# Performance work log

Measured on AMD Instinct MI355X. Metric: run time of the kernel, lower is better.

The kernel has to match this reference:

```python
import jax, jax.numpy as jnp
import numpy as np

DIM = 128
N = 4096


def setup_inputs() -> dict:
    key = jax.random.key(0)
    ks = jax.random.split(key, 12)
    d = DIM
    s = 0.02
    inp = jax.random.normal(ks[0], (N, 2 * d), dtype=jnp.float32)
    # H = myLinear: (2d -> 5d -> 1), tanh after each layer
    Hw1 = jax.random.normal(ks[1], (2 * d, 5 * d), dtype=jnp.float32) * s
    Hb1 = jax.random.normal(ks[2], (5 * d,), dtype=jnp.float32) * s
    Hw2 = jax.random.normal(ks[3], (5 * d, 1), dtype=jnp.float32) * s
    Hb2 = jax.random.normal(ks[4], (1,), dtype=jnp.float32) * s
    # augment_f: (d -> 4d -> 8d -> d*d), tanh after each layer
    Aw1 = jax.random.normal(ks[5], (d, 4 * d), dtype=jnp.float32) * s
    Ab1 = jax.random.normal(ks[6], (4 * d,), dtype=jnp.float32) * s
    Aw2 = jax.random.normal(ks[7], (4 * d, 8 * d), dtype=jnp.float32) * s
    Ab2 = jax.random.normal(ks[8], (8 * d,), dtype=jnp.float32) * s
    Aw3 = jax.random.normal(ks[9], (8 * d, d * d), dtype=jnp.float32) * s
    Ab3 = jax.random.normal(ks[10], (d * d,), dtype=jnp.float32) * s
    u = jax.random.uniform(ks[11], (d,), dtype=jnp.float32, minval=-0.001, maxval=0.001)
    return {"t": 0, "inp": inp, "Hw1": Hw1, "Hb1": Hb1, "Hw2": Hw2, "Hb2": Hb2,
            "Aw1": Aw1, "Ab1": Ab1, "Aw2": Aw2, "Ab2": Ab2, "Aw3": Aw3, "Ab3": Ab3, "u": u}


def reference(t, inp, Hw1, Hb1, Hw2, Hb2, Aw1, Ab1, Aw2, Ab2, Aw3, Ab3, u):
    d = DIM
    n = inp.shape[0]

    def H_scalar(z):  # z: [2d] -> scalar
        h = jnp.tanh(z @ Hw1 + Hb1)
        return jnp.tanh(h @ Hw2 + Hb2)[0]

    # per-sample gradient of scalar H w.r.t. input (== batch_jacobian squeeze)
    g = jax.vmap(jax.grad(H_scalar))(inp)  # [N, 2d]
    dx = g[:, :d]
    dv = -g[:, d:]

    x = inp[:, :d]
    h1 = jnp.tanh(x @ Aw1 + Ab1)            # [N, 4d]
    h2 = jnp.tanh(h1 @ Aw2 + Ab2)           # [N, 8d]
    gq = jnp.tanh(h2 @ Aw3 + Ab3).reshape(n, d, d)  # [N, d, d]
    dv = dv + jnp.einsum("nij,j->ni", gq, u)
    return jnp.concatenate([dx, dv], axis=-1)  # [N, 2d]
```

## Files before the change

### kernel.cpp

```cpp
#include <hip/hip_runtime.h>
#include <hip/hip_bf16.h>
#include <cstdint>


typedef __bf16 bf16_t;
typedef __bf16 bf16x4_t __attribute__((ext_vector_type(4)));
typedef __bf16 bf16x8_t __attribute__((ext_vector_type(8)));
typedef float f32x4_t __attribute__((ext_vector_type(4)));
typedef float f32x16_t __attribute__((ext_vector_type(16)));
typedef int intx4_t __attribute__((ext_vector_type(4)));
typedef int intx8_t __attribute__((ext_vector_type(8)));

#define DIMD 128
#define NROW 4096
#define SMEM_BYTES 18432
#define SMEM3_BYTES 26624

__device__ __forceinline__ float fast_tanh(float x) {
  float t = __builtin_amdgcn_exp2f(x * 2.8853900817779268f);
  return 1.f - 2.f * __builtin_amdgcn_rcpf(t + 1.f);
}

__device__ __forceinline__ uint8_t to_fp8(float x) {
  return (uint8_t)(__builtin_amdgcn_cvt_pk_fp8_f32(x, x, 0, false) & 0xff);
}

__device__ __forceinline__ void g2l16(const void* gp, void* lp) {
  __builtin_amdgcn_global_load_lds(
      reinterpret_cast<__attribute__((address_space(1))) void*>(
          reinterpret_cast<uintptr_t>(gp)),
      reinterpret_cast<__attribute__((address_space(3))) void*>(
          reinterpret_cast<uintptr_t>(lp)),
      16, 0, 0);
}

template <int EPI>
__device__ __forceinline__ void gemm_body(char* smem, int bx, int by,
                                          const bf16_t* A, int lda,
                                          const bf16_t* B, int ldb, int K,
                                          const float* bias, void* outp,
                                          int ldo) {
  constexpr int BK = 32;
  bf16_t* As = (bf16_t*)smem;
  bf16_t* Bs = As + 4096;

  const int m0 = bx * 128;
  const int n0 = by * 128;
  const int tid = threadIdx.x;
  const int wave = tid >> 6;
  const int lane = tid & 63;
  const int wm = wave >> 1;
  const int wn = wave & 1;

  const int sr = lane >> 2;
  const int sk = (((lane & 3) ^ ((sr >> 1) & 3)) * 8);
  const int fr = lane & 15;
  const int fk = (((lane >> 4) ^ ((fr >> 1) & 3)) * 8);

  f32x4_t acc[4][4] = {};

  for (int k0 = 0; k0 < K; k0 += BK) {
    if (k0) __syncthreads();
#pragma unroll
    for (int t = 0; t < 2; ++t) {
      const int rb = wave * 32 + t * 16;
      g2l16(A + (size_t)(m0 + rb + sr) * lda + (k0 + sk), As + rb * BK);
      g2l16(B + (size_t)(n0 + rb + sr) * ldb + (k0 + sk), Bs + rb * BK);
    }
    __syncthreads();

    bf16x8_t af[4], bb[4];
#pragma unroll
    for (int t = 0; t < 4; ++t) {
      af[t] = *(const bf16x8_t*)(As + (wm * 64 + t * 16 + fr) * BK + fk);
      bb[t] = *(const bf16x8_t*)(Bs + (wn * 64 + t * 16 + fr) * BK + fk);
    }
#pragma unroll
    for (int i = 0; i < 4; ++i)
#pragma unroll
      for (int j = 0; j < 4; ++j)
        acc[i][j] = __builtin_amdgcn_mfma_f32_16x16x32_bf16(af[i], bb[j],
                                                            acc[i][j], 0, 0, 0);
  }

  if constexpr (EPI == 0) {
    bf16_t* O = (bf16_t*)outp;
#pragma unroll
    for (int i = 0; i < 4; ++i) {
      const int row = m0 + wm * 64 + i * 16 + (lane >> 4) * 4;
#pragma unroll
      for (int j = 0; j < 4; ++j) {
        const int col = n0 + wn * 64 + j * 16 + fr;
        const float b = bias[col];
#pragma unroll
        for (int r = 0; r < 4; ++r)
          O[(size_t)(row + r) * ldo + col] = (bf16_t)fast_tanh(acc[i][j][r] + b);
      }
    }
  } else if constexpr (EPI == 1) {
    float* O = (float*)outp;
    const bool dx = (n0 < DIMD);
#pragma unroll
    for (int i = 0; i < 4; ++i) {
      const int row = m0 + wm * 64 + i * 16 + (lane >> 4) * 4;
#pragma unroll
      for (int j = 0; j < 4; ++j) {
        const int col = n0 + wn * 64 + j * 16 + fr;
#pragma unroll
        for (int r = 0; r < 4; ++r) {
          const size_t idx = (size_t)(row + r) * ldo + col;
          if (dx) O[idx] = acc[i][j][r];
          else atomicAdd(&O[idx], -acc[i][j][r]);
        }
      }
    }
  } else {
    uint8_t* O = (uint8_t*)outp;
#pragma unroll
    for (int i = 0; i < 4; ++i) {
      const int row = m0 + wm * 64 + i * 16 + (lane >> 4) * 4;
#pragma unroll
      for (int j = 0; j < 4; ++j) {
        const int col = n0 + wn * 64 + j * 16 + fr;
        const float b = bias[col];
#pragma unroll
        for (int r = 0; r < 4; ++r)
          O[(size_t)(row + r) * ldo + col] =
              to_fp8(64.f * fast_tanh(acc[i][j][r] + b));
      }
    }
  }
}

__device__ __forceinline__ void a3_body(char* smem, int bx, int by,
                                        const uint8_t* A, const uint8_t* B,
                                        float* out, const float* ab3,
                                        const float* uvec) {
  constexpr int BK = 64, K = 1024;
  uint8_t* As = (uint8_t*)smem;
  uint8_t* Bs = As + 16384;
  float* red = (float*)(smem + 24576);
  float* us = red + 256;
  float* a3s = us + 128;

  const int m0 = bx * 256;
  const int n0 = by * 128;
  const int tid = threadIdx.x;
  const int wave = tid >> 6;
  const int lane = tid & 63;

  red[tid] = 0.f;
  if (tid < 128) {
    us[tid] = uvec[tid];
    a3s[tid] = ab3[n0 + tid];
  }

  const int sr = lane >> 2;
  const int sk = ((lane & 3) ^ ((sr >> 1) & 3)) * 16;

  const int rl = lane & 31;
  const int w = (rl >> 1) & 3;
  const int c0 = lane >> 5;
  const int sLo = ((2 * c0) ^ w) * 16;
  const int sHi = ((2 * c0 + 1) ^ w) * 16;

  f32x16_t acc[2][4] = {};

  for (int k0 = 0; k0 < K; k0 += BK) {
    if (k0) __syncthreads();
#pragma unroll
    for (int t = 0; t < 4; ++t) {
      const int rb = t * 64 + wave * 16;
      g2l16(A + (size_t)(m0 + rb + sr) * K + (k0 + sk), As + rb * BK);
    }
#pragma unroll
    for (int t = 0; t < 2; ++t) {
      const int rb = t * 64 + wave * 16;
      g2l16(B + (size_t)(n0 + rb + sr) * K + (k0 + sk), Bs + rb * BK);
    }
    __syncthreads();

    intx8_t af[2], bfr[4];
#pragma unroll
    for (int i = 0; i < 2; ++i) {
      const int ra = (wave * 64 + i * 32 + rl) * BK;
      intx4_t lo = *(const intx4_t*)(As + ra + sLo);
      intx4_t hi = *(const intx4_t*)(As + ra + sHi);
      af[i] = __builtin_shufflevector(lo, hi, 0, 1, 2, 3, 4, 5, 6, 7);
    }
#pragma unroll
    for (int j = 0; j < 4; ++j) {
      const int rb2 = (j * 32 + rl) * BK;
      intx4_t lob = *(const intx4_t*)(Bs + rb2 + sLo);
      intx4_t hib = *(const intx4_t*)(Bs + rb2 + sHi);
      bfr[j] = __builtin_shufflevector(lob, hib, 0, 1, 2, 3, 4, 5, 6, 7);
    }
#pragma unroll
    for (int i = 0; i < 2; ++i)
#pragma unroll
      for (int j = 0; j < 4; ++j)
        acc[i][j] = __builtin_amdgcn_mfma_scale_f32_32x32x64_f8f6f4(
            af[i], bfr[j], acc[i][j], 0, 0, 0, 0x79797979, 0, 0x79797979);
  }

  const int q = lane >> 5;
#pragma unroll
  for (int i = 0; i < 2; ++i) {
    float sums[16];
#pragma unroll
    for (int r = 0; r < 16; ++r) sums[r] = 0.f;
#pragma unroll
    for (int j = 0; j < 4; ++j) {
      const int c = j * 32 + rl;
      const float uu = us[c];
      const float b3 = a3s[c];
#pragma unroll
      for (int r = 0; r < 16; ++r) sums[r] += fast_tanh(acc[i][j][r] + b3) * uu;
    }
#pragma unroll
    for (int d = 1; d < 32; d <<= 1)
#pragma unroll
      for (int r = 0; r < 16; ++r) sums[r] += __shfl_xor(sums[r], d, 64);
    if (rl == 0) {
      const int rowb = wave * 64 + i * 32 + 4 * q;
#pragma unroll
      for (int r = 0; r < 16; ++r)
        atomicAdd(&red[rowb + (r & 3) + 8 * (r >> 2)], sums[r]);
    }
  }
  __syncthreads();
  atomicAdd(&out[(size_t)(m0 + tid) * 256 + 128 + by], red[tid]);
}

__device__ __forceinline__ void tcvt_body(char* smem, const float* in,
                                          bf16_t* out, int R, int C, int bx,
                                          int by) {
  float(*t)[33] = (float(*)[33])smem;
  const int c0 = bx * 32;
  const int r0 = by * 32;
  const int tx = threadIdx.x & 31;
  const int ty = threadIdx.x >> 5;
#pragma unroll
  for (int k = 0; k < 4; ++k)
    t[ty + k * 8][tx] = in[(size_t)(r0 + ty + k * 8) * C + c0 + tx];
  __syncthreads();
#pragma unroll
  for (int k = 0; k < 4; ++k)
    out[(size_t)(c0 + ty + k * 8) * R + r0 + tx] = (bf16_t)t[tx][ty + k * 8];
}

__device__ __forceinline__ void aw3t_body(char* smem, const float* Aw3,
                                          uint8_t* Aw3T8, int b) {
  float(*t)[33] = (float(*)[33])smem;
  const int c0 = (b & 511) * 32;
  const int r0 = (b >> 9) * 32;
  const int tx = threadIdx.x & 31;
  const int ty = threadIdx.x >> 5;
#pragma unroll
  for (int k = 0; k < 4; ++k)
    t[ty + k * 8][tx] = Aw3[(size_t)(r0 + ty + k * 8) * 16384 + c0 + tx];
  __syncthreads();
  const int cl = threadIdx.x >> 3;
  const int j = (threadIdx.x & 7) * 4;
  uchar4 v;
  v.x = to_fp8(64.f * t[j + 0][cl]);
  v.y = to_fp8(64.f * t[j + 1][cl]);
  v.z = to_fp8(64.f * t[j + 2][cl]);
  v.w = to_fp8(64.f * t[j + 3][cl]);
  *(uchar4*)(Aw3T8 + (size_t)(c0 + cl) * 1024 + r0 + j) = v;
}

__device__ __forceinline__ void hgrad_row(int row, const bf16_t* h,
                                          const float* Hw2, const float* Hb2,
                                          bf16_t* wout) {
  const int lane = threadIdx.x & 63;
  float hv[10], wv[10];
  float pre2 = 0.f;
#pragma unroll
  for (int t = 0; t < 10; ++t) {
    const int j = lane + t * 64;
    hv[t] = (float)h[(size_t)row * 640 + j];
    wv[t] = Hw2[j];
    pre2 += hv[t] * wv[t];
  }
#pragma unroll
  for (int d = 1; d < 64; d <<= 1) pre2 += __shfl_xor(pre2, d, 64);
  const float y = fast_tanh(pre2 + Hb2[0]);
  const float s = 1.f - y * y;
#pragma unroll
  for (int t = 0; t < 10; ++t) {
    const int j = lane + t * 64;
    wout[(size_t)row * 640 + j] = (bf16_t)(s * wv[t] * (1.f - hv[t] * hv[t]));
  }
}

__global__ __launch_bounds__(256) void launch0(
    const float* __restrict__ inp, bf16_t* __restrict__ inp_bf,
    const float* __restrict__ Hw1, bf16_t* __restrict__ Hw1T,
    const float* __restrict__ Aw1, bf16_t* __restrict__ Aw1T) {
  __shared__ __align__(16) char smem[4224];
  int b = blockIdx.x;
  if (b < 1024) {
    const int i = b * 256 + threadIdx.x;
    const float4 v = ((const float4*)inp)[i];
    bf16x4_t o = {(bf16_t)v.x, (bf16_t)v.y, (bf16_t)v.z, (bf16_t)v.w};
    ((bf16x4_t*)inp_bf)[i] = o;
  } else if (b < 1184) {
    int s = b - 1024;
    tcvt_body(smem, Hw1, Hw1T, 256, 640, s % 20, s / 20);
  } else {
    int s = b - 1184;
    tcvt_body(smem, Aw1, Aw1T, 128, 512, s % 16, s / 16);
  }
}

__global__ __launch_bounds__(256) void launch1(
    const bf16_t* __restrict__ inp_bf, const bf16_t* __restrict__ Hw1T,
    const float* __restrict__ Hb1, bf16_t* __restrict__ h_bf,
    const bf16_t* __restrict__ Aw1T, const float* __restrict__ Ab1,
    bf16_t* __restrict__ h1_bf, const float* __restrict__ Aw2,
    bf16_t* __restrict__ Aw2T, const float* __restrict__ Hw1,
    bf16_t* __restrict__ Hw1_bf, const float* __restrict__ Aw3,
    uint8_t* __restrict__ Aw3T8) {
  __shared__ __align__(16) char smem[SMEM_BYTES];
  const int b = blockIdx.x;
  if (b < 160) {
    gemm_body<0>(smem, b % 32, b / 32, inp_bf, 256, Hw1T, 256, 256, Hb1, h_bf, 640);
  } else if (b < 288) {
    const int i = b - 160;
    gemm_body<0>(smem, i % 32, i / 32, inp_bf, 256, Aw1T, 128, 128, Ab1, h1_bf, 512);
  } else if (b < 800) {
    const int s = b - 288;
    tcvt_body(smem, Aw2, Aw2T, 512, 1024, s % 32, s / 32);
  } else if (b < 960) {
    const int i = (b - 800) * 256 + threadIdx.x;
    const float4 v = ((const float4*)Hw1)[i];
    bf16x4_t o = {(bf16_t)v.x, (bf16_t)v.y, (bf16_t)v.z, (bf16_t)v.w};
    ((bf16x4_t*)Hw1_bf)[i] = o;
  } else {
    aw3t_body(smem, Aw3, Aw3T8, b - 960);
  }
}

__global__ __launch_bounds__(256) void launch2(
    const bf16_t* __restrict__ h1_bf, const bf16_t* __restrict__ Aw2T,
    const float* __restrict__ Ab2, uint8_t* __restrict__ h2_f8,
    const bf16_t* __restrict__ h_bf, const float* __restrict__ Hw2,
    const float* __restrict__ Hb2, bf16_t* __restrict__ w_bf,
    float* __restrict__ out, const float* __restrict__ Aw3,
    uint8_t* __restrict__ Aw3T8) {
  __shared__ __align__(16) char smem[SMEM_BYTES];
  const int b = blockIdx.x;
  if (b < 256) {
    gemm_body<3>(smem, b % 32, b / 32, h1_bf, 512, Aw2T, 512, 512, Ab2, h2_f8, 1024);
  } else if (b < 1280) {
    const int row = (b - 256) * 4 + (threadIdx.x >> 6);
    hgrad_row(row, h_bf, Hw2, Hb2, w_bf);
  } else if (b < 2304) {
    const int i = (b - 1280) * 256 + threadIdx.x;
    ((float4*)out)[i] = make_float4(0.f, 0.f, 0.f, 0.f);
  } else {
    aw3t_body(smem, Aw3, Aw3T8, 8192 + (b - 2304));
  }
}

__global__ __launch_bounds__(256) void launch3(
    const bf16_t* __restrict__ w_bf, const bf16_t* __restrict__ Hw1_bf,
    float* __restrict__ out, const uint8_t* __restrict__ h2_f8,
    const uint8_t* __restrict__ Aw3T8, const float* __restrict__ Ab3,
    const float* __restrict__ uvec) {
  __shared__ __align__(16) char smem[SMEM3_BYTES];
  const int b = blockIdx.x;
  if (b < 64) {
    gemm_body<1>(smem, b % 32, b / 32, w_bf, 640, Hw1_bf, 640, 640, nullptr, out, 256);
  } else {
    const int i = b - 64;
    a3_body(smem, i & 15, i >> 4, h2_f8, Aw3T8, out, Ab3, uvec);
  }
}

extern "C" void kernel_launch(void* const* d_in, const int* in_sizes, int n_in,
                              void* d_out, int out_size, void* d_ws,
                              size_t ws_size, hipStream_t stream) {
  (void)in_sizes; (void)n_in; (void)out_size; (void)ws_size;
  const float* inp = (const float*)d_in[1];
  const float* Hw1 = (const float*)d_in[2];
  const float* Hb1 = (const float*)d_in[3];
  const float* Hw2 = (const float*)d_in[4];
  const float* Hb2 = (const float*)d_in[5];
  const float* Aw1 = (const float*)d_in[6];
  const float* Ab1 = (const float*)d_in[7];
  const float* Aw2 = (const float*)d_in[8];
  const float* Ab2 = (const float*)d_in[9];
  const float* Aw3 = (const float*)d_in[10];
  const float* Ab3 = (const float*)d_in[11];
  const float* u = (const float*)d_in[12];
  float* out = (float*)d_out;

  char* ws = (char*)d_ws;
  bf16_t* inp_bf = (bf16_t*)ws;   ws += (size_t)NROW * 256 * 2;
  bf16_t* Hw1_bf = (bf16_t*)ws;   ws += (size_t)256 * 640 * 2;
  bf16_t* Hw1T = (bf16_t*)ws;     ws += (size_t)640 * 256 * 2;
  bf16_t* Aw1T = (bf16_t*)ws;     ws += (size_t)512 * 128 * 2;
  bf16_t* Aw2T = (bf16_t*)ws;     ws += (size_t)1024 * 512 * 2;
  uint8_t* Aw3T8 = (uint8_t*)ws;  ws += (size_t)16384 * 1024;
  bf16_t* h_bf = (bf16_t*)ws;     ws += (size_t)NROW * 640 * 2;
  bf16_t* w_bf = (bf16_t*)ws;     ws += (size_t)NROW * 640 * 2;
  bf16_t* h1_bf = (bf16_t*)ws;    ws += (size_t)NROW * 512 * 2;
  uint8_t* h2_f8 = (uint8_t*)ws;  ws += (size_t)NROW * 1024;

  launch0<<<1248, 256, 0, stream>>>(inp, inp_bf, Hw1, Hw1T, Aw1, Aw1T);
  launch1<<<9152, 256, 0, stream>>>(inp_bf, Hw1T, Hb1, h_bf, Aw1T, Ab1, h1_bf,
                                    Aw2, Aw2T, Hw1, Hw1_bf, Aw3, Aw3T8);
  launch2<<<10496, 256, 0, stream>>>(h1_bf, Aw2T, Ab2, h2_f8, h_bf, Hw2, Hb2,
                                     w_bf, out, Aw3, Aw3T8);
  launch3<<<2112, 256, 0, stream>>>(w_bf, Hw1_bf, out, h2_f8, Aw3T8, Ab3, u);
}
```

Baseline: 252.9 us.

## Double-buffer fp8 Aw3 GEMM loads and rebalance work across launches

The fp8 Aw3 GEMM main loop now double-buffers its A/B tiles in LDS. The next K-slice is prefetched with global_load_lds while the current one feeds the MFMAs, and each iteration uses one barrier instead of two. The output zeroing moves into launch0, and all Aw3 transpose/convert blocks move into launch1, so launch2 only holds the Aw2 GEMM and the H-gradient rows. Doubling LDS per block in launch3 may reduce occupancy, and launch1 grows much larger.

```diff
diff --git a/kernel.cpp b/kernel.cpp
--- a/kernel.cpp
+++ b/kernel.cpp
@@ -14,7 +14,7 @@
 #define DIMD 128
 #define NROW 4096
 #define SMEM_BYTES 18432
-#define SMEM3_BYTES 26624
+#define SMEM3_BYTES 51200
 
 __device__ __forceinline__ float fast_tanh(float x) {
   float t = __builtin_amdgcn_exp2f(x * 2.8853900817779268f);
@@ -136,10 +136,10 @@
                                         const uint8_t* A, const uint8_t* B,
                                         float* out, const float* ab3,
                                         const float* uvec) {
-  constexpr int BK = 64, K = 1024;
+  constexpr int BK = 64, K = 1024, NIT = K / BK;
   uint8_t* As = (uint8_t*)smem;
-  uint8_t* Bs = As + 16384;
-  float* red = (float*)(smem + 24576);
+  uint8_t* Bs = (uint8_t*)smem + 32768;
+  float* red = (float*)(smem + 49152);
   float* us = red + 256;
   float* a3s = us + 128;
 
@@ -157,6 +157,8 @@
 
   const int sr = lane >> 2;
   const int sk = ((lane & 3) ^ ((sr >> 1) & 3)) * 16;
+  const uint8_t* pA = A + (size_t)(m0 + wave * 16 + sr) * K + sk;
+  const uint8_t* pB = B + (size_t)(n0 + wave * 16 + sr) * K + sk;
 
   const int rl = lane & 31;
   const int w = (rl >> 1) & 3;
@@ -166,33 +168,38 @@
 
   f32x16_t acc[2][4] = {};
 
-  for (int k0 = 0; k0 < K; k0 += BK) {
-    if (k0) __syncthreads();
-#pragma unroll
-    for (int t = 0; t < 4; ++t) {
-      const int rb = t * 64 + wave * 16;
-      g2l16(A + (size_t)(m0 + rb + sr) * K + (k0 + sk), As + rb * BK);
-    }
-#pragma unroll
-    for (int t = 0; t < 2; ++t) {
-      const int rb = t * 64 + wave * 16;
-      g2l16(B + (size_t)(n0 + rb + sr) * K + (k0 + sk), Bs + rb * BK);
-    }
+  auto stage = [&](int kk, int buf) {
+    uint8_t* Ad = As + buf * 16384 + wave * 16 * BK;
+    uint8_t* Bd = Bs + buf * 8192 + wave * 16 * BK;
+#pragma unroll
+    for (int t = 0; t < 4; ++t)
+      g2l16(pA + (size_t)t * 64 * K + kk, Ad + t * 64 * BK);
+#pragma unroll
+    for (int t = 0; t < 2; ++t)
+      g2l16(pB + (size_t)t * 64 * K + kk, Bd + t * 64 * BK);
+  };
+
+  stage(0, 0);
+#pragma unroll 2
+  for (int it = 0; it < NIT; ++it) {
     __syncthreads();
-
+    if (it + 1 < NIT) stage((it + 1) * BK, (it + 1) & 1);
+
+    const uint8_t* Ac = As + (it & 1) * 16384;
+    const uint8_t* Bc = Bs + (it & 1) * 8192;
     intx8_t af[2], bfr[4];
 #pragma unroll
     for (int i = 0; i < 2; ++i) {
       const int ra = (wave * 64 + i * 32 + rl) * BK;
-      intx4_t lo = *(const intx4_t*)(As + ra + sLo);
-      intx4_t hi = *(const intx4_t*)(As + ra + sHi);
+      intx4_t lo = *(const intx4_t*)(Ac + ra + sLo);
+      intx4_t hi = *(const intx4_t*)(Ac + ra + sHi);
       af[i] = __builtin_shufflevector(lo, hi, 0, 1, 2, 3, 4, 5, 6, 7);
     }
 #pragma unroll
     for (int j = 0; j < 4; ++j) {
       const int rb2 = (j * 32 + rl) * BK;
-      intx4_t lob = *(const intx4_t*)(Bs + rb2 + sLo);
-      intx4_t hib = *(const intx4_t*)(Bs + rb2 + sHi);
+      intx4_t lob = *(const intx4_t*)(Bc + rb2 + sLo);
+      intx4_t hib = *(const intx4_t*)(Bc + rb2 + sHi);
       bfr[j] = __builtin_shufflevector(lob, hib, 0, 1, 2, 3, 4, 5, 6, 7);
     }
 #pragma unroll
@@ -297,7 +304,8 @@
 __global__ __launch_bounds__(256) void launch0(
     const float* __restrict__ inp, bf16_t* __restrict__ inp_bf,
     const float* __restrict__ Hw1, bf16_t* __restrict__ Hw1T,
-    const float* __restrict__ Aw1, bf16_t* __restrict__ Aw1T) {
+    const float* __restrict__ Aw1, bf16_t* __restrict__ Aw1T,
+    float* __restrict__ out) {
   __shared__ __align__(16) char smem[4224];
   int b = blockIdx.x;
   if (b < 1024) {
@@ -308,9 +316,12 @@
   } else if (b < 1184) {
     int s = b - 1024;
     tcvt_body(smem, Hw1, Hw1T, 256, 640, s % 20, s / 20);
-  } else {
+  } else if (b < 1248) {
     int s = b - 1184;
     tcvt_body(smem, Aw1, Aw1T, 128, 512, s % 16, s / 16);
+  } else {
+    const int i = (b - 1248) * 256 + threadIdx.x;
+    ((float4*)out)[i] = make_float4(0.f, 0.f, 0.f, 0.f);
   }
 }
 
@@ -346,21 +357,14 @@
     const bf16_t* __restrict__ h1_bf, const bf16_t* __restrict__ Aw2T,
     const float* __restrict__ Ab2, uint8_t* __restrict__ h2_f8,
     const bf16_t* __restrict__ h_bf, const float* __restrict__ Hw2,
-    const float* __restrict__ Hb2, bf16_t* __restrict__ w_bf,
-    float* __restrict__ out, const float* __restrict__ Aw3,
-    uint8_t* __restrict__ Aw3T8) {
+    const float* __restrict__ Hb2, bf16_t* __restrict__ w_bf) {
   __shared__ __align__(16) char smem[SMEM_BYTES];
   const int b = blockIdx.x;
   if (b < 256) {
     gemm_body<3>(smem, b % 32, b / 32, h1_bf, 512, Aw2T, 512, 512, Ab2, h2_f8, 1024);
-  } else if (b < 1280) {
+  } else {
     const int row = (b - 256) * 4 + (threadIdx.x >> 6);
     hgrad_row(row, h_bf, Hw2, Hb2, w_bf);
-  } else if (b < 2304) {
-    const int i = (b - 1280) * 256 + threadIdx.x;
-    ((float4*)out)[i] = make_float4(0.f, 0.f, 0.f, 0.f);
-  } else {
-    aw3t_body(smem, Aw3, Aw3T8, 8192 + (b - 2304));
   }
 }
 
@@ -409,10 +413,10 @@
   bf16_t* h1_bf = (bf16_t*)ws;    ws += (size_t)NROW * 512 * 2;
   uint8_t* h2_f8 = (uint8_t*)ws;  ws += (size_t)NROW * 1024;
 
-  launch0<<<1248, 256, 0, stream>>>(inp, inp_bf, Hw1, Hw1T, Aw1, Aw1T);
-  launch1<<<9152, 256, 0, stream>>>(inp_bf, Hw1T, Hb1, h_bf, Aw1T, Ab1, h1_bf,
-                                    Aw2, Aw2T, Hw1, Hw1_bf, Aw3, Aw3T8);
-  launch2<<<10496, 256, 0, stream>>>(h1_bf, Aw2T, Ab2, h2_f8, h_bf, Hw2, Hb2,
-                                     w_bf, out, Aw3, Aw3T8);
+  launch0<<<2272, 256, 0, stream>>>(inp, inp_bf, Hw1, Hw1T, Aw1, Aw1T, out);
+  launch1<<<17344, 256, 0, stream>>>(inp_bf, Hw1T, Hb1, h_bf, Aw1T, Ab1, h1_bf,
+                                     Aw2, Aw2T, Hw1, Hw1_bf, Aw3, Aw3T8);
+  launch2<<<1280, 256, 0, stream>>>(h1_bf, Aw2T, Ab2, h2_f8, h_bf, Hw2, Hb2,
+                                    w_bf);
   launch3<<<2112, 256, 0, stream>>>(w_bf, Hw1_bf, out, h2_f8, Aw3T8, Ab3, u);
 }
```

New measurement: 280.3 us. +10.9%, slower.

## Fuse fp32-to-bf16 input conversion into GEMM staging and rebalance launch work

Applied to the files above, without the earlier changes.

The GEMMs now load fp32 operands (inp, Hw1) directly and convert them to bf16 while writing to shared memory, so the separate inp_bf and Hw1_bf conversion passes and their workspace buffers go away. The Aw2 transpose and output zeroing move to the first launch, and all Aw3 fp8 transposition is consolidated into launch1. The a3 block index mapping is also swapped. Staging through registers instead of async global-to-LDS loads may add latency inside the GEMM loops.

```diff
diff --git a/kernel.cpp b/kernel.cpp
--- a/kernel.cpp
+++ b/kernel.cpp
@@ -34,10 +34,28 @@
       16, 0, 0);
 }
 
-template <int EPI>
+__device__ __forceinline__ void stage_f32(const float* __restrict__ src,
+                                          int lda_e, int r0, int k0,
+                                          bf16_t* dst) {
+  const int tid = threadIdx.x;
+  const int r = tid >> 1;
+  const int kc0 = (tid & 1) * 2;
+  const float* p = src + (size_t)(r0 + r) * lda_e + k0;
+#pragma unroll
+  for (int cc = 0; cc < 2; ++cc) {
+    const int c = kc0 + cc;
+    const float4 v0 = *(const float4*)(p + c * 8);
+    const float4 v1 = *(const float4*)(p + c * 8 + 4);
+    bf16x8_t w = {(bf16_t)v0.x, (bf16_t)v0.y, (bf16_t)v0.z, (bf16_t)v0.w,
+                  (bf16_t)v1.x, (bf16_t)v1.y, (bf16_t)v1.z, (bf16_t)v1.w};
+    *(bf16x8_t*)(dst + r * 32 + ((c ^ ((r >> 1) & 3)) * 8)) = w;
+  }
+}
+
+template <int EPI, bool AF32, bool BF32>
 __device__ __forceinline__ void gemm_body(char* smem, int bx, int by,
-                                          const bf16_t* A, int lda,
-                                          const bf16_t* B, int ldb, int K,
+                                          const void* Ap, int lda,
+                                          const void* Bp, int ldb, int K,
                                           const float* bias, void* outp,
                                           int ldo) {
   constexpr int BK = 32;
@@ -61,11 +79,25 @@
 
   for (int k0 = 0; k0 < K; k0 += BK) {
     if (k0) __syncthreads();
-#pragma unroll
-    for (int t = 0; t < 2; ++t) {
-      const int rb = wave * 32 + t * 16;
-      g2l16(A + (size_t)(m0 + rb + sr) * lda + (k0 + sk), As + rb * BK);
-      g2l16(B + (size_t)(n0 + rb + sr) * ldb + (k0 + sk), Bs + rb * BK);
+    if constexpr (AF32) {
+      stage_f32((const float*)Ap, lda, m0, k0, As);
+    } else {
+      const bf16_t* A = (const bf16_t*)Ap;
+#pragma unroll
+      for (int t = 0; t < 2; ++t) {
+        const int rb = wave * 32 + t * 16;
+        g2l16(A + (size_t)(m0 + rb + sr) * lda + (k0 + sk), As + rb * BK);
+      }
+    }
+    if constexpr (BF32) {
+      stage_f32((const float*)Bp, ldb, n0, k0, Bs);
+    } else {
+      const bf16_t* B = (const bf16_t*)Bp;
+#pragma unroll
+      for (int t = 0; t < 2; ++t) {
+        const int rb = wave * 32 + t * 16;
+        g2l16(B + (size_t)(n0 + rb + sr) * ldb + (k0 + sk), Bs + rb * BK);
+      }
     }
     __syncthreads();
 
@@ -295,50 +327,43 @@
 }
 
 __global__ __launch_bounds__(256) void launch0(
-    const float* __restrict__ inp, bf16_t* __restrict__ inp_bf,
     const float* __restrict__ Hw1, bf16_t* __restrict__ Hw1T,
-    const float* __restrict__ Aw1, bf16_t* __restrict__ Aw1T) {
+    const float* __restrict__ Aw1, bf16_t* __restrict__ Aw1T,
+    const float* __restrict__ Aw2, bf16_t* __restrict__ Aw2T,
+    float* __restrict__ out) {
   __shared__ __align__(16) char smem[4224];
   int b = blockIdx.x;
-  if (b < 1024) {
-    const int i = b * 256 + threadIdx.x;
-    const float4 v = ((const float4*)inp)[i];
-    bf16x4_t o = {(bf16_t)v.x, (bf16_t)v.y, (bf16_t)v.z, (bf16_t)v.w};
-    ((bf16x4_t*)inp_bf)[i] = o;
-  } else if (b < 1184) {
-    int s = b - 1024;
-    tcvt_body(smem, Hw1, Hw1T, 256, 640, s % 20, s / 20);
+  if (b < 160) {
+    tcvt_body(smem, Hw1, Hw1T, 256, 640, b % 20, b / 20);
+  } else if (b < 224) {
+    int s = b - 160;
+    tcvt_body(smem, Aw1, Aw1T, 128, 512, s % 16, s / 16);
+  } else if (b < 736) {
+    int s = b - 224;
+    tcvt_body(smem, Aw2, Aw2T, 512, 1024, s % 32, s / 32);
   } else {
-    int s = b - 1184;
-    tcvt_body(smem, Aw1, Aw1T, 128, 512, s % 16, s / 16);
+    const int i = (b - 736) * 256 + threadIdx.x;
+    ((float4*)out)[i] = make_float4(0.f, 0.f, 0.f, 0.f);
   }
 }
 
 __global__ __launch_bounds__(256) void launch1(
-    const bf16_t* __restrict__ inp_bf, const bf16_t* __restrict__ Hw1T,
+    const float* __restrict__ inp, const bf16_t* __restrict__ Hw1T,
     const float* __restrict__ Hb1, bf16_t* __restrict__ h_bf,
     const bf16_t* __restrict__ Aw1T, const float* __restrict__ Ab1,
-    bf16_t* __restrict__ h1_bf, const float* __restrict__ Aw2,
-    bf16_t* __restrict__ Aw2T, const float* __restrict__ Hw1,
-    bf16_t* __restrict__ Hw1_bf, const float* __restrict__ Aw3,
+    bf16_t* __restrict__ h1_bf, const float* __restrict__ Aw3,
     uint8_t* __restrict__ Aw3T8) {
   __shared__ __align__(16) char smem[SMEM_BYTES];
   const int b = blockIdx.x;
   if (b < 160) {
-    gemm_body<0>(smem, b % 32, b / 32, inp_bf, 256, Hw1T, 256, 256, Hb1, h_bf, 640);
+    gemm_body<0, true, false>(smem, b % 32, b / 32, inp, 256, Hw1T, 256, 256,
+                              Hb1, h_bf, 640);
   } else if (b < 288) {
     const int i = b - 160;
-    gemm_body<0>(smem, i % 32, i / 32, inp_bf, 256, Aw1T, 128, 128, Ab1, h1_bf, 512);
-  } else if (b < 800) {
-    const int s = b - 288;
-    tcvt_body(smem, Aw2, Aw2T, 512, 1024, s % 32, s / 32);
-  } else if (b < 960) {
-    const int i = (b - 800) * 256 + threadIdx.x;
-    const float4 v = ((const float4*)Hw1)[i];
-    bf16x4_t o = {(bf16_t)v.x, (bf16_t)v.y, (bf16_t)v.z, (bf16_t)v.w};
-    ((bf16x4_t*)Hw1_bf)[i] = o;
+    gemm_body<0, true, false>(smem, i % 32, i / 32, inp, 256, Aw1T, 128, 128,
+                              Ab1, h1_bf, 512);
   } else {
-    aw3t_body(smem, Aw3, Aw3T8, b - 960);
+    aw3t_body(smem, Aw3, Aw3T8, b - 288);
   }
 }
 
@@ -346,36 +371,31 @@
     const bf16_t* __restrict__ h1_bf, const bf16_t* __restrict__ Aw2T,
     const float* __restrict__ Ab2, uint8_t* __restrict__ h2_f8,
     const bf16_t* __restrict__ h_bf, const float* __restrict__ Hw2,
-    const float* __restrict__ Hb2, bf16_t* __restrict__ w_bf,
-    float* __restrict__ out, const float* __restrict__ Aw3,
-    uint8_t* __restrict__ Aw3T8) {
+    const float* __restrict__ Hb2, bf16_t* __restrict__ w_bf) {
   __shared__ __align__(16) char smem[SMEM_BYTES];
   const int b = blockIdx.x;
   if (b < 256) {
-    gemm_body<3>(smem, b % 32, b / 32, h1_bf, 512, Aw2T, 512, 512, Ab2, h2_f8, 1024);
-  } else if (b < 1280) {
+    gemm_body<3, false, false>(smem, b % 32, b / 32, h1_bf, 512, Aw2T, 512,
+                               512, Ab2, h2_f8, 1024);
+  } else {
     const int row = (b - 256) * 4 + (threadIdx.x >> 6);
     hgrad_row(row, h_bf, Hw2, Hb2, w_bf);
-  } else if (b < 2304) {
-    const int i = (b - 1280) * 256 + threadIdx.x;
-    ((float4*)out)[i] = make_float4(0.f, 0.f, 0.f, 0.f);
-  } else {
-    aw3t_body(smem, Aw3, Aw3T8, 8192 + (b - 2304));
   }
 }
 
 __global__ __launch_bounds__(256) void launch3(
-    const bf16_t* __restrict__ w_bf, const bf16_t* __restrict__ Hw1_bf,
+    const bf16_t* __restrict__ w_bf, const float* __restrict__ Hw1,
     float* __restrict__ out, const uint8_t* __restrict__ h2_f8,
     const uint8_t* __restrict__ Aw3T8, const float* __restrict__ Ab3,
     const float* __restrict__ uvec) {
   __shared__ __align__(16) char smem[SMEM3_BYTES];
   const int b = blockIdx.x;
   if (b < 64) {
-    gemm_body<1>(smem, b % 32, b / 32, w_bf, 640, Hw1_bf, 640, 640, nullptr, out, 256);
+    gemm_body<1, false, true>(smem, b % 32, b / 32, w_bf, 640, Hw1, 640, 640,
+                              nullptr, out, 256);
   } else {
     const int i = b - 64;
-    a3_body(smem, i & 15, i >> 4, h2_f8, Aw3T8, out, Ab3, uvec);
+    a3_body(smem, i >> 7, i & 127, h2_f8, Aw3T8, out, Ab3, uvec);
   }
 }
 
@@ -398,8 +418,6 @@
   float* out = (float*)d_out;
 
   char* ws = (char*)d_ws;
-  bf16_t* inp_bf = (bf16_t*)ws;   ws += (size_t)NROW * 256 * 2;
-  bf16_t* Hw1_bf = (bf16_t*)ws;   ws += (size_t)256 * 640 * 2;
   bf16_t* Hw1T = (bf16_t*)ws;     ws += (size_t)640 * 256 * 2;
   bf16_t* Aw1T = (bf16_t*)ws;     ws += (size_t)512 * 128 * 2;
   bf16_t* Aw2T = (bf16_t*)ws;     ws += (size_t)1024 * 512 * 2;
@@ -409,10 +427,10 @@
   bf16_t* h1_bf = (bf16_t*)ws;    ws += (size_t)NROW * 512 * 2;
   uint8_t* h2_f8 = (uint8_t*)ws;  ws += (size_t)NROW * 1024;
 
-  launch0<<<1248, 256, 0, stream>>>(inp, inp_bf, Hw1, Hw1T, Aw1, Aw1T);
-  launch1<<<9152, 256, 0, stream>>>(inp_bf, Hw1T, Hb1, h_bf, Aw1T, Ab1, h1_bf,
-                                    Aw2, Aw2T, Hw1, Hw1_bf, Aw3, Aw3T8);
-  launch2<<<10496, 256, 0, stream>>>(h1_bf, Aw2T, Ab2, h2_f8, h_bf, Hw2, Hb2,
-                                     w_bf, out, Aw3, Aw3T8);
-  launch3<<<2112, 256, 0, stream>>>(w_bf, Hw1_bf, out, h2_f8, Aw3T8, Ab3, u);
-}
+  launch0<<<1760, 256, 0, stream>>>(Hw1, Hw1T, Aw1, Aw1T, Aw2, Aw2T, out);
+  launch1<<<16672, 256, 0, stream>>>(inp, Hw1T, Hb1, h_bf, Aw1T, Ab1, h1_bf,
+                                     Aw3, Aw3T8);
+  launch2<<<1280, 256, 0, stream>>>(h1_bf, Aw2T, Ab2, h2_f8, h_bf, Hw2, Hb2,
+                                    w_bf);
+  launch3<<<2112, 256, 0, stream>>>(w_bf, Hw1, out, h2_f8, Aw3T8, Ab3, u);
+}
```

Result: slower. 273.0 us (+7.9%).

## Shrink GEMM tiles to 64x64 and move weight conversions into first launch

Applied to the files above, without the earlier changes.

Replaces the 128x128 bf16 GEMM tile with a 64x64 tile (each wave computes 2x2 MFMA blocks), which quadruples the number of GEMM blocks in launches 1-3 for better CU occupancy and load balance. The Aw2 transpose, the Hw1 bf16 conversion and the zeroing of the output buffer move from launches 1 and 2 into launch0. This leaves the later launches dominated by GEMM and Aw3 work and shrinks their shared-memory footprint. The trade-off is lower per-tile data reuse and more global loads per FLOP.

```diff
diff --git a/kernel.cpp b/kernel.cpp
--- a/kernel.cpp
+++ b/kernel.cpp
@@ -13,7 +13,7 @@
 
 #define DIMD 128
 #define NROW 4096
-#define SMEM_BYTES 18432
+#define SMEM_G64 8192
 #define SMEM3_BYTES 26624
 
 __device__ __forceinline__ float fast_tanh(float x) {
@@ -35,17 +35,17 @@
 }
 
 template <int EPI>
-__device__ __forceinline__ void gemm_body(char* smem, int bx, int by,
-                                          const bf16_t* A, int lda,
-                                          const bf16_t* B, int ldb, int K,
-                                          const float* bias, void* outp,
-                                          int ldo) {
+__device__ __forceinline__ void gemm64_body(char* smem, int bx, int by,
+                                            const bf16_t* A, int lda,
+                                            const bf16_t* B, int ldb, int K,
+                                            const float* bias, void* outp,
+                                            int ldo) {
   constexpr int BK = 32;
   bf16_t* As = (bf16_t*)smem;
-  bf16_t* Bs = As + 4096;
-
-  const int m0 = bx * 128;
-  const int n0 = by * 128;
+  bf16_t* Bs = As + 2048;
+
+  const int m0 = bx * 64;
+  const int n0 = by * 64;
   const int tid = threadIdx.x;
   const int wave = tid >> 6;
   const int lane = tid & 63;
@@ -57,71 +57,52 @@
   const int fr = lane & 15;
   const int fk = (((lane >> 4) ^ ((fr >> 1) & 3)) * 8);
 
-  f32x4_t acc[4][4] = {};
+  f32x4_t acc[2][2] = {};
 
   for (int k0 = 0; k0 < K; k0 += BK) {
     if (k0) __syncthreads();
+    const int rb = wave * 16;
+    g2l16(A + (size_t)(m0 + rb + sr) * lda + (k0 + sk), As + rb * BK);
+    g2l16(B + (size_t)(n0 + rb + sr) * ldb + (k0 + sk), Bs + rb * BK);
+    __syncthreads();
+
+    bf16x8_t af[2], bb[2];
 #pragma unroll
     for (int t = 0; t < 2; ++t) {
-      const int rb = wave * 32 + t * 16;
-      g2l16(A + (size_t)(m0 + rb + sr) * lda + (k0 + sk), As + rb * BK);
-      g2l16(B + (size_t)(n0 + rb + sr) * ldb + (k0 + sk), Bs + rb * BK);
-    }
-    __syncthreads();
-
-    bf16x8_t af[4], bb[4];
-#pragma unroll
-    for (int t = 0; t < 4; ++t) {
-      af[t] = *(const bf16x8_t*)(As + (wm * 64 + t * 16 + fr) * BK + fk);
-      bb[t] = *(const bf16x8_t*)(Bs + (wn * 64 + t * 16 + fr) * BK + fk);
-    }
-#pragma unroll
-    for (int i = 0; i < 4; ++i)
-#pragma unroll
-      for (int j = 0; j < 4; ++j)
+      af[t] = *(const bf16x8_t*)(As + (wm * 32 + t * 16 + fr) * BK + fk);
+      bb[t] = *(const bf16x8_t*)(Bs + (wn * 32 + t * 16 + fr) * BK + fk);
+    }
+#pragma unroll
+    for (int i = 0; i < 2; ++i)
+#pragma unroll
+      for (int j = 0; j < 2; ++j)
         acc[i][j] = __builtin_amdgcn_mfma_f32_16x16x32_bf16(af[i], bb[j],
                                                             acc[i][j], 0, 0, 0);
   }
 
-  if constexpr (EPI == 0) {
-    bf16_t* O = (bf16_t*)outp;
-#pragma unroll
-    for (int i = 0; i < 4; ++i) {
-      const int row = m0 + wm * 64 + i * 16 + (lane >> 4) * 4;
-#pragma unroll
-      for (int j = 0; j < 4; ++j) {
-        const int col = n0 + wn * 64 + j * 16 + fr;
+#pragma unroll
+  for (int i = 0; i < 2; ++i) {
+    const int row = m0 + wm * 32 + i * 16 + (lane >> 4) * 4;
+#pragma unroll
+    for (int j = 0; j < 2; ++j) {
+      const int col = n0 + wn * 32 + j * 16 + fr;
+      if constexpr (EPI == 0) {
+        bf16_t* O = (bf16_t*)outp;
         const float b = bias[col];
 #pragma unroll
         for (int r = 0; r < 4; ++r)
           O[(size_t)(row + r) * ldo + col] = (bf16_t)fast_tanh(acc[i][j][r] + b);
-      }
-    }
-  } else if constexpr (EPI == 1) {
-    float* O = (float*)outp;
-    const bool dx = (n0 < DIMD);
-#pragma unroll
-    for (int i = 0; i < 4; ++i) {
-      const int row = m0 + wm * 64 + i * 16 + (lane >> 4) * 4;
-#pragma unroll
-      for (int j = 0; j < 4; ++j) {
-        const int col = n0 + wn * 64 + j * 16 + fr;
+      } else if constexpr (EPI == 1) {
+        float* O = (float*)outp;
+        const bool dx = (n0 < DIMD);
 #pragma unroll
         for (int r = 0; r < 4; ++r) {
           const size_t idx = (size_t)(row + r) * ldo + col;
           if (dx) O[idx] = acc[i][j][r];
           else atomicAdd(&O[idx], -acc[i][j][r]);
         }
-      }
-    }
-  } else {
-    uint8_t* O = (uint8_t*)outp;
-#pragma unroll
-    for (int i = 0; i < 4; ++i) {
-      const int row = m0 + wm * 64 + i * 16 + (lane >> 4) * 4;
-#pragma unroll
-      for (int j = 0; j < 4; ++j) {
-        const int col = n0 + wn * 64 + j * 16 + fr;
+      } else {
+        uint8_t* O = (uint8_t*)outp;
         const float b = bias[col];
 #pragma unroll
         for (int r = 0; r < 4; ++r)
@@ -297,7 +278,9 @@
 __global__ __launch_bounds__(256) void launch0(
     const float* __restrict__ inp, bf16_t* __restrict__ inp_bf,
     const float* __restrict__ Hw1, bf16_t* __restrict__ Hw1T,
-    const float* __restrict__ Aw1, bf16_t* __restrict__ Aw1T) {
+    bf16_t* __restrict__ Hw1_bf, const float* __restrict__ Aw1,
+    bf16_t* __restrict__ Aw1T, const float* __restrict__ Aw2,
+    bf16_t* __restrict__ Aw2T, float* __restrict__ out) {
   __shared__ __align__(16) char smem[4224];
   int b = blockIdx.x;
   if (b < 1024) {
@@ -308,9 +291,20 @@
   } else if (b < 1184) {
     int s = b - 1024;
     tcvt_body(smem, Hw1, Hw1T, 256, 640, s % 20, s / 20);
-  } else {
+  } else if (b < 1248) {
     int s = b - 1184;
     tcvt_body(smem, Aw1, Aw1T, 128, 512, s % 16, s / 16);
+  } else if (b < 1760) {
+    int s = b - 1248;
+    tcvt_body(smem, Aw2, Aw2T, 512, 1024, s % 32, s / 32);
+  } else if (b < 1920) {
+    const int i = (b - 1760) * 256 + threadIdx.x;
+    const float4 v = ((const float4*)Hw1)[i];
+    bf16x4_t o = {(bf16_t)v.x, (bf16_t)v.y, (bf16_t)v.z, (bf16_t)v.w};
+    ((bf16x4_t*)Hw1_bf)[i] = o;
+  } else {
+    const int i = (b - 1920) * 256 + threadIdx.x;
+    ((float4*)out)[i] = make_float4(0.f, 0.f, 0.f, 0.f);
   }
 }
 
@@ -318,27 +312,19 @@
     const bf16_t* __restrict__ inp_bf, const bf16_t* __restrict__ Hw1T,
     const float* __restrict__ Hb1, bf16_t* __restrict__ h_bf,
     const bf16_t* __restrict__ Aw1T, const float* __restrict__ Ab1,
-    bf16_t* __restrict__ h1_bf, const float* __restrict__ Aw2,
-    bf16_t* __restrict__ Aw2T, const float* __restrict__ Hw1,
-    bf16_t* __restrict__ Hw1_bf, const float* __restrict__ Aw3,
+    bf16_t* __restrict__ h1_bf, const float* __restrict__ Aw3,
     uint8_t* __restrict__ Aw3T8) {
-  __shared__ __align__(16) char smem[SMEM_BYTES];
+  __shared__ __align__(16) char smem[SMEM_G64];
   const int b = blockIdx.x;
-  if (b < 160) {
-    gemm_body<0>(smem, b % 32, b / 32, inp_bf, 256, Hw1T, 256, 256, Hb1, h_bf, 640);
-  } else if (b < 288) {
-    const int i = b - 160;
-    gemm_body<0>(smem, i % 32, i / 32, inp_bf, 256, Aw1T, 128, 128, Ab1, h1_bf, 512);
-  } else if (b < 800) {
-    const int s = b - 288;
-    tcvt_body(smem, Aw2, Aw2T, 512, 1024, s % 32, s / 32);
-  } else if (b < 960) {
-    const int i = (b - 800) * 256 + threadIdx.x;
-    const float4 v = ((const float4*)Hw1)[i];
-    bf16x4_t o = {(bf16_t)v.x, (bf16_t)v.y, (bf16_t)v.z, (bf16_t)v.w};
-    ((bf16x4_t*)Hw1_bf)[i] = o;
+  if (b < 640) {
+    gemm64_body<0>(smem, b % 64, b / 64, inp_bf, 256, Hw1T, 256, 256, Hb1,
+                   h_bf, 640);
+  } else if (b < 1152) {
+    const int i = b - 640;
+    gemm64_body<0>(smem, i % 64, i / 64, inp_bf, 256, Aw1T, 128, 128, Ab1,
+                   h1_bf, 512);
   } else {
-    aw3t_body(smem, Aw3, Aw3T8, b - 960);
+    aw3t_body(smem, Aw3, Aw3T8, b - 1152);
   }
 }
 
@@ -347,20 +333,17 @@
     const float* __restrict__ Ab2, uint8_t* __restrict__ h2_f8,
     const bf16_t* __restrict__ h_bf, const float* __restrict__ Hw2,
     const float* __restrict__ Hb2, bf16_t* __restrict__ w_bf,
-    float* __restrict__ out, const float* __restrict__ Aw3,
-    uint8_t* __restrict__ Aw3T8) {
-  __shared__ __align__(16) char smem[SMEM_BYTES];
+    const float* __restrict__ Aw3, uint8_t* __restrict__ Aw3T8) {
+  __shared__ __align__(16) char smem[SMEM_G64];
   const int b = blockIdx.x;
-  if (b < 256) {
-    gemm_body<3>(smem, b % 32, b / 32, h1_bf, 512, Aw2T, 512, 512, Ab2, h2_f8, 1024);
-  } else if (b < 1280) {
-    const int row = (b - 256) * 4 + (threadIdx.x >> 6);
+  if (b < 1024) {
+    gemm64_body<3>(smem, b % 64, b / 64, h1_bf, 512, Aw2T, 512, 512, Ab2,
+                   h2_f8, 1024);
+  } else if (b < 2048) {
+    const int row = (b - 1024) * 4 + (threadIdx.x >> 6);
     hgrad_row(row, h_bf, Hw2, Hb2, w_bf);
-  } else if (b < 2304) {
-    const int i = (b - 1280) * 256 + threadIdx.x;
-    ((float4*)out)[i] = make_float4(0.f, 0.f, 0.f, 0.f);
   } else {
-    aw3t_body(smem, Aw3, Aw3T8, 8192 + (b - 2304));
+    aw3t_body(smem, Aw3, Aw3T8, 8192 + (b - 2048));
   }
 }
 
@@ -371,10 +354,11 @@
     const float* __restrict__ uvec) {
   __shared__ __align__(16) char smem[SMEM3_BYTES];
   const int b = blockIdx.x;
-  if (b < 64) {
-    gemm_body<1>(smem, b % 32, b / 32, w_bf, 640, Hw1_bf, 640, 640, nullptr, out, 256);
+  if (b < 256) {
+    gemm64_body<1>(smem, b % 64, b / 64, w_bf, 640, Hw1_bf, 640, 640, nullptr,
+                   out, 256);
   } else {
-    const int i = b - 64;
+    const int i = b - 256;
     a3_body(smem, i & 15, i >> 4, h2_f8, Aw3T8, out, Ab3, uvec);
   }
 }
@@ -409,10 +393,11 @@
   bf16_t* h1_bf = (bf16_t*)ws;    ws += (size_t)NROW * 512 * 2;
   uint8_t* h2_f8 = (uint8_t*)ws;  ws += (size_t)NROW * 1024;
 
-  launch0<<<1248, 256, 0, stream>>>(inp, inp_bf, Hw1, Hw1T, Aw1, Aw1T);
-  launch1<<<9152, 256, 0, stream>>>(inp_bf, Hw1T, Hb1, h_bf, Aw1T, Ab1, h1_bf,
-                                    Aw2, Aw2T, Hw1, Hw1_bf, Aw3, Aw3T8);
-  launch2<<<10496, 256, 0, stream>>>(h1_bf, Aw2T, Ab2, h2_f8, h_bf, Hw2, Hb2,
-                                     w_bf, out, Aw3, Aw3T8);
-  launch3<<<2112, 256, 0, stream>>>(w_bf, Hw1_bf, out, h2_f8, Aw3T8, Ab3, u);
-}
+  launch0<<<2944, 256, 0, stream>>>(inp, inp_bf, Hw1, Hw1T, Hw1_bf, Aw1, Aw1T,
+                                    Aw2, Aw2T, out);
+  launch1<<<9344, 256, 0, stream>>>(inp_bf, Hw1T, Hb1, h_bf, Aw1T, Ab1, h1_bf,
+                                    Aw3, Aw3T8);
+  launch2<<<10240, 256, 0, stream>>>(h1_bf, Aw2T, Ab2, h2_f8, h_bf, Hw2, Hb2,
+                                     w_bf, Aw3, Aw3T8);
+  launch3<<<2304, 256, 0, stream>>>(w_bf, Hw1_bf, out, h2_f8, Aw3T8, Ab3, u);
+}
```

Measured after the change: 250.4 us. No clear change (-1.0%).
